# Kernel optimization log

Measured on AMD Instinct MI355X. Metric: run time of the kernel, lower is better.

## Reference

```python
import jax, jax.numpy as jnp
import numpy as np

B, C, H, W = 8, 64, 256, 256
EPS = 1e-5


def setup_inputs() -> dict:
    key = jax.random.key(0)
    ks = jax.random.split(key, 8)
    s = 1.0 / np.sqrt(C)
    return {
        "x": jax.random.normal(ks[0], (B, C, H, W), dtype=jnp.float32),
        "Wq": jax.random.uniform(ks[1], (C, C), jnp.float32, -s, s),
        "bq": jnp.zeros((C,), jnp.float32),
        "Wk": jax.random.uniform(ks[2], (C, C), jnp.float32, -s, s),
        "bk": jnp.zeros((C,), jnp.float32),
        "Wv": jax.random.uniform(ks[3], (C, C), jnp.float32, -s, s),
        "bv": jnp.zeros((C,), jnp.float32),
        "gamma": jnp.ones((C,), jnp.float32),
        "beta": jnp.zeros((C,), jnp.float32),
        "running_mean": jnp.zeros((C,), jnp.float32),
        "running_var": jnp.ones((C,), jnp.float32),
        "alpha": jnp.full((1,), 0.25, jnp.float32),  # PReLU single shared parameter
    }


def _conv1x1(x, w, b):
    # 1x1 conv == per-pixel channel mixing: [B,Ci,H,W] x [Co,Ci] -> [B,Co,H,W]
    return jnp.einsum("bihw,oi->bohw", x, w) + b[None, :, None, None]


def reference(x, Wq, bq, Wk, bk, Wv, bv, gamma, beta, running_mean, running_var, alpha):
    # d_k = sqrt(H); scores scaled by d_k**0.5 -> H**0.25 (faithful to source)
    scale = jnp.asarray(H, x.dtype) ** 0.25
    Q = _conv1x1(x, Wq, bq)
    K = _conv1x1(x, Wk, bk)
    V = _conv1x1(x, Wv, bv)
    # scores over spatial rows: [B,C,H,H]
    scores = jnp.einsum("bchw,bcgw->bchg", Q, K) / scale
    attn = jax.nn.softmax(scores, axis=-1)
    out = jnp.einsum("bchg,bcgw->bchw", attn, V)
    # BatchNorm2d (eval mode: running stats), then PReLU; dropout is identity in eval
    inv = gamma / jnp.sqrt(running_var + EPS)
    out = out * inv[None, :, None, None] + (beta - running_mean * inv)[None, :, None, None]
    a = alpha[0]
    out = jnp.where(out >= 0, out, a * out)
    return out
```

## Files before the change

kernel.cpp:

```cpp
#include <hip/hip_runtime.h>

#define B_ 8
#define C_ 64
#define H_ 256
#define W_ 256
#define HW_ 65536
#define PLANE_ 33554432

typedef __attribute__((ext_vector_type(8))) short short8;
typedef __attribute__((ext_vector_type(4))) float f32x4;
typedef __attribute__((ext_vector_type(4))) unsigned short ushort4v;

__device__ __forceinline__ unsigned short f2bf(float f){
  unsigned u = __float_as_uint(f);
  u += 0x7fffu + ((u >> 16) & 1u);
  return (unsigned short)(u >> 16);
}

__global__ __launch_bounds__(256) void proj_kernel(
    const float* __restrict__ x,
    const float* __restrict__ Wq, const float* __restrict__ bq,
    const float* __restrict__ Wk, const float* __restrict__ bk,
    const float* __restrict__ Wv, const float* __restrict__ bv,
    unsigned short* __restrict__ Qb, unsigned short* __restrict__ Kb,
    unsigned short* __restrict__ Vb)
{
  __shared__ unsigned short Xt[W_*64];
  const int tid = threadIdx.x;
  const int lane = tid & 63;
  const int wv  = tid >> 6;
  const int q4 = lane >> 4, l16 = lane & 15;
  const int bid = blockIdx.x;
  const int b = bid >> 8, h = bid & 255;

  const float* wsrc[3] = {Wq, Wk, Wv};
  const float* bsrc[3] = {bq, bk, bv};

  {
    const float* xb = x + (size_t)b*C_*HW_ + (size_t)h*W_;
    #pragma unroll
    for (int it=0; it<16; ++it){
      int i = it*4 + wv;
      float4 v = *(const float4*)(xb + (size_t)i*HW_ + lane*4);
      float fv[4] = {v.x, v.y, v.z, v.w};
      #pragma unroll
      for (int k2=0;k2<4;++k2){
        int w = lane*4 + k2;
        int slot = (w&7) ^ ((w>>3)&7);
        Xt[w*64 + (i ^ (slot<<3))] = f2bf(fv[k2]);
      }
    }
  }

  float bias[3][4];
  #pragma unroll
  for (int p=0;p<3;++p)
    #pragma unroll
    for (int nf=0;nf<4;++nf)
      bias[p][nf] = bsrc[p][nf*16 + l16];

  __syncthreads();

  short8 aX[4][2];
  #pragma unroll
  for (int mf=0;mf<4;++mf){
    int w = wv*64 + mf*16 + l16;
    int slot = (w&7) ^ ((w>>3)&7);
    #pragma unroll
    for (int kk=0;kk<2;++kk)
      aX[mf][kk] = *(const short8*)&Xt[w*64 + ((8*q4 + 32*kk) ^ (slot<<3))];
  }
  __syncthreads();

  unsigned short* Wl = Xt;
  #pragma unroll
  for (int it=0; it<12; ++it){
    int idx4 = it*256 + tid;
    int p = idx4 >> 10;
    int rem = idx4 & 1023;
    int o = rem >> 4, i4 = rem & 15;
    float4 v = *(const float4*)(wsrc[p] + o*64 + i4*4);
    ushort4v sv;
    sv[0]=f2bf(v.x); sv[1]=f2bf(v.y); sv[2]=f2bf(v.z); sv[3]=f2bf(v.w);
    *(ushort4v*)&Wl[p*4096 + o*64 + ((i4*4) ^ ((o&7)<<3))] = sv;
  }
  __syncthreads();

  unsigned short* outp[3] = {Qb, Kb, Vb};
  const size_t obase = (size_t)b*C_*HW_ + (size_t)h*W_;

  #pragma unroll
  for (int p=0;p<3;++p){
    unsigned short* op = outp[p];
    #pragma unroll
    for (int nf=0;nf<4;++nf){
      const int o = nf*16 + l16;
      const int key = (o&7)<<3;
      short8 bW0 = *(const short8*)&Wl[p*4096 + o*64 + ((8*q4)      ^ key)];
      short8 bW1 = *(const short8*)&Wl[p*4096 + o*64 + ((8*q4 + 32) ^ key)];
      f32x4 acc[4];
      #pragma unroll
      for (int mf=0;mf<4;++mf){ f32x4 z={0.f,0.f,0.f,0.f}; acc[mf]=z; }
      #pragma unroll
      for (int mf=0;mf<4;++mf)
        acc[mf] = __builtin_amdgcn_mfma_f32_16x16x32_bf16(aX[mf][0], bW0, acc[mf], 0,0,0);
      #pragma unroll
      for (int mf=0;mf<4;++mf)
        acc[mf] = __builtin_amdgcn_mfma_f32_16x16x32_bf16(aX[mf][1], bW1, acc[mf], 0,0,0);
      const float bb = bias[p][nf];
      #pragma unroll
      for (int mf=0;mf<4;++mf){
        ushort4v sv;
        #pragma unroll
        for (int r=0;r<4;++r) sv[r] = f2bf(acc[mf][r] + bb);
        *(ushort4v*)&op[obase + (size_t)o*HW_ + (wv*64 + mf*16 + 4*q4)] = sv;
      }
    }
  }
}

__global__ __launch_bounds__(256) void transpose_v(unsigned short* __restrict__ Vb)
{
  const int pi[10] = {0,0,0,0,1,1,1,2,2,3};
  const int pj[10] = {0,1,2,3,1,2,3,2,3,3};
  __shared__ unsigned short tA[64*72];
  __shared__ unsigned short tB[64*72];
  int t = threadIdx.x;
  int bid = blockIdx.x;
  int bc = bid / 10, pr = bid - bc*10;
  int ti = pi[pr], tj = pj[pr];
  unsigned short* base = Vb + (size_t)bc*HW_;
  int diag = (ti == tj);
  #pragma unroll
  for (int k=0;k<2;++k){
    int flat = t + k*256;
    int i = flat >> 3, j = (flat & 7)*8;
    int4 va = *(const int4*)(base + (size_t)(ti*64+i)*256 + tj*64 + j);
    *(int4*)&tA[i*72 + j] = va;
    if (!diag){
      int4 vb2 = *(const int4*)(base + (size_t)(tj*64+i)*256 + ti*64 + j);
      *(int4*)&tB[i*72 + j] = vb2;
    }
  }
  __syncthreads();
  #pragma unroll
  for (int k=0;k<2;++k){
    int flat = t + k*256;
    int i = flat >> 3, j = (flat & 7)*8;
    int4 vo; unsigned short* po = (unsigned short*)&vo;
    #pragma unroll
    for (int e=0;e<8;++e) po[e] = tA[(j+e)*72 + i];
    *(int4*)(base + (size_t)(tj*64+i)*256 + ti*64 + j) = vo;
    if (!diag){
      int4 vo2; unsigned short* po2 = (unsigned short*)&vo2;
      #pragma unroll
      for (int e=0;e<8;++e) po2[e] = tB[(j+e)*72 + i];
      *(int4*)(base + (size_t)(ti*64+i)*256 + tj*64 + j) = vo2;
    }
  }
}

__device__ __forceinline__ int swzkey(int r){ return (r & 31) ^ ((r & 3) << 3); }

__device__ __forceinline__ void stage_tile(unsigned short* dst, const unsigned short* src, int tid){
  #pragma unroll
  for (int k=0;k<8;++k){
    int j = tid + k*256;
    int gj = j ^ swzkey(j >> 5);
    __builtin_amdgcn_global_load_lds(
      (const __attribute__((address_space(1))) void*)(src + (size_t)gj*8),
      (__attribute__((address_space(3))) void*)(dst + (size_t)j*8),
      16, 0, 0);
  }
}

__global__ __launch_bounds__(256) void attn_kernel(
    const unsigned short* __restrict__ Qb, const unsigned short* __restrict__ Kb,
    const unsigned short* __restrict__ Vtb,
    const float* __restrict__ gamma, const float* __restrict__ beta,
    const float* __restrict__ rmean, const float* __restrict__ rvar,
    const float* __restrict__ alphaP,
    float* __restrict__ out)
{
  __shared__ unsigned short s[64*256];
  const int tid = threadIdx.x;
  const int lane = tid & 63;
  const int wv = tid >> 6;
  const int q4 = lane >> 4, l16 = lane & 15;
  const int n = blockIdx.x;
  const int work = (n & 7)*256 + (n >> 3);
  const int bc = work >> 2, ht = work & 3;
  const int c = bc & 63;

  const unsigned short* Qp = Qb  + (size_t)bc*HW_ + (size_t)ht*64*W_;
  const unsigned short* Kp = Kb  + (size_t)bc*HW_;
  const unsigned short* Vp = Vtb + (size_t)bc*HW_;

  stage_tile(s, Kp, tid);

  short8 aq[8];
  {
    const int row = wv*16 + l16;
    #pragma unroll
    for (int kk=0;kk<8;++kk)
      aq[kk] = *(const short8*)(Qp + (size_t)row*W_ + 8*q4 + 32*kk);
  }

  f32x4 sa[16];
  #pragma unroll
  for (int f=0;f<16;++f){ f32x4 z={0.f,0.f,0.f,0.f}; sa[f]=z; }

  __syncthreads();
  #pragma unroll
  for (int gt=0; gt<4; ++gt){
    #pragma unroll
    for (int nf=0;nf<4;++nf){
      const int g = nf*16 + l16;
      const int ko = swzkey(g);
      const int f = gt*4 + nf;
      #pragma unroll
      for (int kk=0;kk<8;++kk){
        short8 bk_ = *(const short8*)&s[g*256 + (((q4 + 4*kk) ^ ko) << 3)];
        sa[f] = __builtin_amdgcn_mfma_f32_16x16x32_bf16(aq[kk], bk_, sa[f], 0,0,0);
      }
    }
    __syncthreads();
    if (gt < 3){
      stage_tile(s, Kp + (size_t)(gt+1)*64*W_, tid);
      __syncthreads();
    }
  }

  float mrow[4], rden[4];
  #pragma unroll
  for (int r=0;r<4;++r){
    float m = -3.0e38f;
    #pragma unroll
    for (int f=0;f<16;++f) m = fmaxf(m, sa[f][r]);
    m = fmaxf(m, __shfl_xor(m, 1, 16));
    m = fmaxf(m, __shfl_xor(m, 2, 16));
    m = fmaxf(m, __shfl_xor(m, 4, 16));
    m = fmaxf(m, __shfl_xor(m, 8, 16));
    mrow[r] = m;
  }
  const float cs = 0.25f * 1.4426950408889634f;
  float psum[4] = {0.f,0.f,0.f,0.f};
  #pragma unroll
  for (int f=0;f<16;++f){
    #pragma unroll
    for (int r=0;r<4;++r){
      float pv = exp2f((sa[f][r] - mrow[r]) * cs);
      sa[f][r] = pv;
      psum[r] += pv;
    }
  }
  #pragma unroll
  for (int r=0;r<4;++r){
    float ssum = psum[r];
    ssum += __shfl_xor(ssum, 1, 16);
    ssum += __shfl_xor(ssum, 2, 16);
    ssum += __shfl_xor(ssum, 4, 16);
    ssum += __shfl_xor(ssum, 8, 16);
    rden[r] = 1.0f / ssum;
  }

  #pragma unroll
  for (int r=0;r<4;++r){
    const int row = wv*16 + 4*q4 + r;
    const int ko = swzkey(row);
    #pragma unroll
    for (int f=0;f<16;++f){
      const int g2 = l16 + 16*f;
      s[row*256 + ((((g2>>3) ^ ko) << 3) | (g2 & 7))] = f2bf(sa[f][r] * rden[r]);
    }
  }
  __syncthreads();

  short8 pb[8];
  {
    const int row = wv*16 + l16;
    const int ko = swzkey(row);
    #pragma unroll
    for (int kk=0;kk<8;++kk)
      pb[kk] = *(const short8*)&s[row*256 + (((q4 + 4*kk) ^ ko) << 3)];
  }
  __syncthreads();

  f32x4 oa[16];
  #pragma unroll
  for (int f=0;f<16;++f){ f32x4 z={0.f,0.f,0.f,0.f}; oa[f]=z; }

  stage_tile(s, Vp, tid);
  __syncthreads();
  #pragma unroll
  for (int wt=0; wt<4; ++wt){
    #pragma unroll
    for (int nf=0;nf<4;++nf){
      const int wrow = nf*16 + l16;
      const int ko = swzkey(wrow);
      const int mw = wt*4 + nf;
      #pragma unroll
      for (int kk=0;kk<8;++kk){
        short8 av = *(const short8*)&s[wrow*256 + (((q4 + 4*kk) ^ ko) << 3)];
        oa[mw] = __builtin_amdgcn_mfma_f32_16x16x32_bf16(av, pb[kk], oa[mw], 0,0,0);
      }
    }
    __syncthreads();
    if (wt < 3){
      stage_tile(s, Vp + (size_t)(wt+1)*64*W_, tid);
      __syncthreads();
    }
  }

  const float inv   = gamma[c] / sqrtf(rvar[c] + 1e-5f);
  const float shift = beta[c] - rmean[c]*inv;
  const float al    = alphaP[0];
  float* ob = out + (size_t)bc*HW_ + (size_t)ht*64*W_;
  const int hrow = wv*16 + l16;
  #pragma unroll
  for (int mw=0; mw<16; ++mw){
    f32x4 v;
    #pragma unroll
    for (int r=0;r<4;++r){
      float t = oa[mw][r]*inv + shift;
      v[r] = (t >= 0.f) ? t : al*t;
    }
    *(f32x4*)&ob[(size_t)hrow*W_ + mw*16 + 4*q4] = v;
  }
}

extern "C" void kernel_launch(void* const* d_in, const int* in_sizes, int n_in,
                              void* d_out, int out_size, void* d_ws, size_t ws_size,
                              hipStream_t stream)
{
  const float* x     = (const float*)d_in[0];
  const float* Wq    = (const float*)d_in[1];
  const float* bq    = (const float*)d_in[2];
  const float* Wk    = (const float*)d_in[3];
  const float* bk    = (const float*)d_in[4];
  const float* Wv    = (const float*)d_in[5];
  const float* bv    = (const float*)d_in[6];
  const float* gamma = (const float*)d_in[7];
  const float* beta  = (const float*)d_in[8];
  const float* rmean = (const float*)d_in[9];
  const float* rvar  = (const float*)d_in[10];
  const float* alpha = (const float*)d_in[11];
  float* out = (float*)d_out;

  unsigned short* Qb = (unsigned short*)d_ws;
  unsigned short* Kb = Qb + (size_t)PLANE_;
  unsigned short* Vb = Kb + (size_t)PLANE_;

  proj_kernel<<<B_*H_, 256, 0, stream>>>(x, Wq,bq, Wk,bk, Wv,bv, Qb, Kb, Vb);
  transpose_v<<<B_*C_*10, 256, 0, stream>>>(Vb);
  attn_kernel<<<B_*C_*4, 256, 0, stream>>>(Qb, Kb, Vb, gamma, beta, rmean, rvar, alpha, out);
}
```

Measured before the change: 417.8 us.

## Stage projection outputs through LDS for coalesced stores and prefetch weights per projection

The projection kernel now issues all x loads into registers before converting, loads only one weight matrix at a time into a separate LDS region, and prefetches the next weight during output staging. Output tiles are written to LDS with an XOR swizzle and then stored to global memory as full contiguous 512-byte rows per wave instead of scattered 8-byte fragments. A launch bound of 4 blocks per SM is added. The aim is better global store coalescing and overlap of weight loads, at the cost of extra LDS traffic, more barriers and higher register pressure from 16 float4 loads held in flight.

```diff
diff --git a/kernel.cpp b/kernel.cpp
--- a/kernel.cpp
+++ b/kernel.cpp
@@ -17,7 +17,7 @@
   return (unsigned short)(u >> 16);
 }
 
-__global__ __launch_bounds__(256) void proj_kernel(
+__global__ __launch_bounds__(256, 4) void proj_kernel(
     const float* __restrict__ x,
     const float* __restrict__ Wq, const float* __restrict__ bq,
     const float* __restrict__ Wk, const float* __restrict__ bk,
@@ -25,7 +25,9 @@
     unsigned short* __restrict__ Qb, unsigned short* __restrict__ Kb,
     unsigned short* __restrict__ Vb)
 {
-  __shared__ unsigned short Xt[W_*64];
+  __shared__ unsigned short lds[W_*64 + 64*64];
+  unsigned short* Xt = lds;
+  unsigned short* Wl = lds + W_*64;
   const int tid = threadIdx.x;
   const int lane = tid & 63;
   const int wv  = tid >> 6;
@@ -36,29 +38,46 @@
   const float* wsrc[3] = {Wq, Wk, Wv};
   const float* bsrc[3] = {bq, bk, bv};
 
-  {
-    const float* xb = x + (size_t)b*C_*HW_ + (size_t)h*W_;
-    #pragma unroll
-    for (int it=0; it<16; ++it){
-      int i = it*4 + wv;
-      float4 v = *(const float4*)(xb + (size_t)i*HW_ + lane*4);
-      float fv[4] = {v.x, v.y, v.z, v.w};
-      #pragma unroll
-      for (int k2=0;k2<4;++k2){
-        int w = lane*4 + k2;
-        int slot = (w&7) ^ ((w>>3)&7);
-        Xt[w*64 + (i ^ (slot<<3))] = f2bf(fv[k2]);
-      }
-    }
-  }
-
-  float bias[3][4];
+  const float* xb = x + (size_t)b*C_*HW_ + (size_t)h*W_;
+  float4 xv[16];
+  #pragma unroll
+  for (int it=0; it<16; ++it){
+    int i = it*4 + wv;
+    xv[it] = *(const float4*)(xb + (size_t)i*HW_ + lane*4);
+  }
+  float4 w0v[4];
+  #pragma unroll
+  for (int k=0;k<4;++k){
+    int idx4 = k*256 + tid;
+    int o = idx4 >> 4, i4 = idx4 & 15;
+    w0v[k] = *(const float4*)(Wq + o*64 + i4*4);
+  }
+  float biasr[3][4];
   #pragma unroll
   for (int p=0;p<3;++p)
     #pragma unroll
     for (int nf=0;nf<4;++nf)
-      bias[p][nf] = bsrc[p][nf*16 + l16];
-
+      biasr[p][nf] = bsrc[p][nf*16 + l16];
+
+  #pragma unroll
+  for (int it=0; it<16; ++it){
+    int i = it*4 + wv;
+    float fv[4] = {xv[it].x, xv[it].y, xv[it].z, xv[it].w};
+    #pragma unroll
+    for (int k2=0;k2<4;++k2){
+      int w = lane*4 + k2;
+      int slot = (w&7) ^ ((w>>3)&7);
+      Xt[w*64 + (i ^ (slot<<3))] = f2bf(fv[k2]);
+    }
+  }
+  #pragma unroll
+  for (int k=0;k<4;++k){
+    int idx4 = k*256 + tid;
+    int o = idx4 >> 4, i4 = idx4 & 15;
+    ushort4v sv;
+    sv[0]=f2bf(w0v[k].x); sv[1]=f2bf(w0v[k].y); sv[2]=f2bf(w0v[k].z); sv[3]=f2bf(w0v[k].w);
+    *(ushort4v*)&Wl[o*64 + ((i4*4) ^ ((o&7)<<3))] = sv;
+  }
   __syncthreads();
 
   short8 aX[4][2];
@@ -70,34 +89,20 @@
     for (int kk=0;kk<2;++kk)
       aX[mf][kk] = *(const short8*)&Xt[w*64 + ((8*q4 + 32*kk) ^ (slot<<3))];
   }
-  __syncthreads();
-
-  unsigned short* Wl = Xt;
-  #pragma unroll
-  for (int it=0; it<12; ++it){
-    int idx4 = it*256 + tid;
-    int p = idx4 >> 10;
-    int rem = idx4 & 1023;
-    int o = rem >> 4, i4 = rem & 15;
-    float4 v = *(const float4*)(wsrc[p] + o*64 + i4*4);
-    ushort4v sv;
-    sv[0]=f2bf(v.x); sv[1]=f2bf(v.y); sv[2]=f2bf(v.z); sv[3]=f2bf(v.w);
-    *(ushort4v*)&Wl[p*4096 + o*64 + ((i4*4) ^ ((o&7)<<3))] = sv;
-  }
-  __syncthreads();
 
   unsigned short* outp[3] = {Qb, Kb, Vb};
   const size_t obase = (size_t)b*C_*HW_ + (size_t)h*W_;
+  unsigned short* Obuf = Xt;
 
   #pragma unroll
   for (int p=0;p<3;++p){
-    unsigned short* op = outp[p];
+    ushort4v pk[4][4];
     #pragma unroll
     for (int nf=0;nf<4;++nf){
       const int o = nf*16 + l16;
       const int key = (o&7)<<3;
-      short8 bW0 = *(const short8*)&Wl[p*4096 + o*64 + ((8*q4)      ^ key)];
-      short8 bW1 = *(const short8*)&Wl[p*4096 + o*64 + ((8*q4 + 32) ^ key)];
+      short8 bW0 = *(const short8*)&Wl[o*64 + ((8*q4)      ^ key)];
+      short8 bW1 = *(const short8*)&Wl[o*64 + ((8*q4 + 32) ^ key)];
       f32x4 acc[4];
       #pragma unroll
       for (int mf=0;mf<4;++mf){ f32x4 z={0.f,0.f,0.f,0.f}; acc[mf]=z; }
@@ -107,14 +112,55 @@
       #pragma unroll
       for (int mf=0;mf<4;++mf)
         acc[mf] = __builtin_amdgcn_mfma_f32_16x16x32_bf16(aX[mf][1], bW1, acc[mf], 0,0,0);
-      const float bb = bias[p][nf];
+      const float bb = biasr[p][nf];
       #pragma unroll
       for (int mf=0;mf<4;++mf){
         ushort4v sv;
         #pragma unroll
         for (int r=0;r<4;++r) sv[r] = f2bf(acc[mf][r] + bb);
-        *(ushort4v*)&op[obase + (size_t)o*HW_ + (wv*64 + mf*16 + 4*q4)] = sv;
-      }
+        pk[nf][mf] = sv;
+      }
+    }
+    float4 wnv[4];
+    if (p < 2){
+      #pragma unroll
+      for (int k=0;k<4;++k){
+        int idx4 = k*256 + tid;
+        int o = idx4 >> 4, i4 = idx4 & 15;
+        wnv[k] = *(const float4*)(wsrc[p+1] + o*64 + i4*4);
+      }
+    }
+    __syncthreads();
+
+    #pragma unroll
+    for (int nf=0;nf<4;++nf){
+      const int o = nf*16 + l16;
+      const int key = (o&7)<<3;
+      #pragma unroll
+      for (int mf=0;mf<4;++mf){
+        int w4 = wv*16 + mf*4 + q4;
+        *(ushort4v*)&Obuf[o*256 + ((w4 ^ key)<<2)] = pk[nf][mf];
+      }
+    }
+    if (p < 2){
+      #pragma unroll
+      for (int k=0;k<4;++k){
+        int idx4 = k*256 + tid;
+        int o = idx4 >> 4, i4 = idx4 & 15;
+        ushort4v sv;
+        sv[0]=f2bf(wnv[k].x); sv[1]=f2bf(wnv[k].y); sv[2]=f2bf(wnv[k].z); sv[3]=f2bf(wnv[k].w);
+        *(ushort4v*)&Wl[o*64 + ((i4*4) ^ ((o&7)<<3))] = sv;
+      }
+    }
+    __syncthreads();
+
+    unsigned short* op = outp[p];
+    #pragma unroll
+    for (int rr=0; rr<16; ++rr){
+      const int o = wv*16 + rr;
+      const int key = (o&7)<<3;
+      ushort4v sv = *(const ushort4v*)&Obuf[o*256 + ((lane ^ key)<<2)];
+      *(ushort4v*)&op[obase + (size_t)o*HW_ + lane*4] = sv;
     }
   }
 }
```

Measured after the change: 423.7 us. No clear change (+1.4%).
